# Kernel optimization log

Hardware: AMD Instinct MI355X
Metric: run time of the kernel (lower is better)

## Reference

```python
import jax, jax.numpy as jnp
import numpy as np

DIM = 256
K = 8192


def setup_inputs() -> dict:
    key = jax.random.key(0)
    k1, k2 = jax.random.split(key)
    x = jax.random.normal(k1, (16, DIM, 32, 32), dtype=jnp.float32)
    # embed buffer initialized uniform(-0.02, 0.02), shape (1, 1, dim, num_embeddings)
    embed = jax.random.uniform(k2, (1, 1, DIM, K), dtype=jnp.float32, minval=-0.02, maxval=0.02)
    return {"x": x, "embed": embed}


def reference(x, embed):
    B, C, H, W = x.shape
    K_ = embed.shape[-1]
    xp = jnp.transpose(x, (0, 2, 3, 1))            # [B,H,W,C]  (size=(1,1) => block reshape is identity)
    flat = xp.reshape(-1, C)                       # [N,C]
    e = embed.reshape(C, K_)                       # [C,K]
    # pairwise squared distances: ||f||^2 - 2 f.e + ||e||^2
    dist = (jnp.sum(flat * flat, axis=1, keepdims=True)
            - 2.0 * (flat @ e)
            + jnp.sum(e * e, axis=0, keepdims=True))  # [N,K]
    ind = jnp.argmin(dist, axis=1)                 # [N] (argmax of -dist)
    # codebook gather
    q = jnp.take(e.T, ind, axis=0).reshape(B, H, W, C)
    # perplexity from one-hot mean
    counts = jnp.zeros((K_,), dtype=jnp.float32).at[ind].add(1.0)
    avg_probs = counts / flat.shape[0]
    perplexity = jnp.exp(-jnp.sum(avg_probs * jnp.log(avg_probs + 1e-10)))
    # commitment loss (egu=False branch): mean((sg(q) - x)^2)
    diff = jnp.mean((jax.lax.stop_gradient(q) - xp) ** 2)
    # straight-through estimator
    q_st = xp + jax.lax.stop_gradient(q - xp)
    quantize = jnp.transpose(q_st, (0, 3, 1, 2))   # [B,C,H,W]
    embed_ind = ind.reshape(B, H, W)
    return quantize, diff, embed_ind, perplexity
```

## Files before the change

### kernel.cpp

```cpp
#include <hip/hip_runtime.h>

typedef _Float16 f16;
typedef f16 half8 __attribute__((ext_vector_type(8)));
typedef float f32x4 __attribute__((ext_vector_type(4)));
typedef unsigned long long u64;
typedef unsigned int u32;
typedef unsigned short u16;

#define KD 8192
#define DIFF_OFF 4194304
#define EIND_OFF 4194305
#define PERP_OFF 4210689
#define LCAP 262144
#define BUFSZ (24 * 512)


__device__ inline u32 umin32(u32 a, u32 b) { return a < b ? a : b; }
__device__ inline u32 umax32(u32 a, u32 b) { return a > b ? a : b; }
__device__ inline u64 pack64(float d, unsigned col) {
  u32 u = __float_as_uint(d);
  u = (u >> 31) ? ~u : (u | 0x80000000u);
  return ((u64)u << 32) | col;
}
__device__ inline void gl16(const f16* g, f16* l) {
  __builtin_amdgcn_global_load_lds(
      (const __attribute__((address_space(1))) void*)g,
      (__attribute__((address_space(3))) void*)l, 16, 0, 0);
}
__device__ inline float exact_d(const float* __restrict__ x, const float* __restrict__ e,
                                int b, int hw, int col, float F, const float* __restrict__ eev) {
  float a = 0.f;
#pragma unroll 8
  for (int c = 0; c < 256; ++c)
    a = fmaf(x[((size_t)(b * 256 + c) << 10) + hw], e[(size_t)c * KD + col], a);
  float t = fmaf(-2.f, a, F);
  return t + eev[col];
}

__global__ __launch_bounds__(256) void k_prep(const float* __restrict__ x,
                                              const float* __restrict__ e,
                                              float* __restrict__ Fv,
                                              float* __restrict__ eev,
                                              u32* __restrict__ eemax,
                                              f16* __restrict__ ehTf,
                                              f16* __restrict__ xhTf) {
#pragma clang fp contract(off)
  __shared__ float sm[64][65];
  const int bid = blockIdx.x, tid = threadIdx.x;
  if (bid < 32) {
    int k = bid * 256 + tid;
    float s = 0.0f;
    for (int c = 0; c < 256; ++c) { float v = e[(size_t)c * KD + k]; float sq = v * v; s = s + sq; }
    eev[k] = s;
    atomicMax(eemax, __float_as_uint(s));
  } else if (bid < 96) {
    int n = (bid - 32) * 256 + tid;
    int b = n >> 10, hw = n & 1023;
    const float* px = x + ((size_t)b << 18) + hw;
    float sblk[2];
#pragma unroll
    for (int blk = 0; blk < 2; ++blk) {
      float r[8];
#pragma unroll
      for (int j = 0; j < 8; ++j) { float v = px[(size_t)(blk * 128 + j) << 10]; r[j] = v * v; }
      for (int i = 8; i < 128; i += 8) {
#pragma unroll
        for (int j = 0; j < 8; ++j) {
          float v = px[(size_t)(blk * 128 + i + j) << 10];
          float sq = v * v;
          r[j] = r[j] + sq;
        }
      }
      sblk[blk] = ((r[0] + r[1]) + (r[2] + r[3])) + ((r[4] + r[5]) + (r[6] + r[7]));
    }
    Fv[n] = sblk[0] + sblk[1];
  } else if (bid < 608) {
    int t = bid - 96;
    int k0 = (t >> 2) * 64, c0 = (t & 3) * 64;
    int tx = tid & 63, ty = tid >> 6;
#pragma unroll
    for (int i = 0; i < 16; ++i) {
      int cl = i * 4 + ty;
      sm[cl][tx] = e[(size_t)(c0 + cl) * KD + k0 + tx];
    }
    __syncthreads();
#pragma unroll
    for (int p = 0; p < 2; ++p) {
      int i = tid + p * 256;
      int kl = i & 63, cg = i >> 6;
      int kkl = cg >> 2, gg = cg & 3;
      int chb = kkl * 32 + gg * 8;
      half8 h;
#pragma unroll
      for (int j = 0; j < 8; ++j) h[j] = (f16)sm[chb + j][kl];
      int tile = (k0 >> 4) + (kl >> 4);
      int kk = (c0 >> 5) + kkl;
      int lanef = gg * 16 + (kl & 15);
      *(half8*)(ehTf + ((size_t)(tile * 8 + kk) * 64 + lanef) * 8) = h;
    }
  } else {
    int t = bid - 608;
    int b = t >> 6, rem = t & 63;
    int hw0 = (rem >> 2) * 64, c0 = (rem & 3) * 64;
    int tx = tid & 63, ty = tid >> 6;
#pragma unroll
    for (int i = 0; i < 16; ++i) {
      int cl = i * 4 + ty;
      sm[cl][tx] = x[((size_t)(b * 256 + c0 + cl) << 10) + hw0 + tx];
    }
    __syncthreads();
#pragma unroll
    for (int p = 0; p < 2; ++p) {
      int i = tid + p * 256;
      int nl = i & 63, cg = i >> 6;
      int kkl = cg >> 2, gg = cg & 3;
      int chb = kkl * 32 + gg * 8;
      half8 h;
#pragma unroll
      for (int j = 0; j < 8; ++j) h[j] = (f16)sm[chb + j][nl];
      int rt = b * 64 + (hw0 >> 4) + (nl >> 4);
      int kk = (c0 >> 5) + kkl;
      int lanef = gg * 16 + (nl & 15);
      *(half8*)(xhTf + ((size_t)(rt * 8 + kk) * 64 + lanef) * 8) = h;
    }
  }
}

__global__ __launch_bounds__(512, 4) void k_gemm(const f16* __restrict__ xhTf,
                                                 const f16* __restrict__ ehTf,
                                                 const float* __restrict__ eev,
                                                 u32* __restrict__ m1,
                                                 u16* __restrict__ m2) {
  __shared__ __align__(16) f16 ldsbuf[3 * BUFSZ];
  __shared__ u32 red1[4][128];
  __shared__ u32 red2[4][128];
  const int tid = threadIdx.x;
  const int lane = tid & 63, w = tid >> 6;
  const int wm = w >> 2, wn = w & 3;
  const int l15 = lane & 15, g = lane >> 4;
  const int colblk = blockIdx.x & 31;
  const int rowblk = (int)blockIdx.x >> 5;

  const int blk0 = w * 3;
  const f16* gsrc[3];
#pragma unroll
  for (int i = 0; i < 3; ++i) {
    int b = blk0 + i;
    gsrc[i] = ((b < 8) ? (xhTf + (size_t)(rowblk * 8 + b) * 4096)
                       : (ehTf + (size_t)(colblk * 16 + (b - 8)) * 4096)) + lane * 8;
  }

  f32x4 acc[4][4];
#pragma unroll
  for (int i = 0; i < 4; ++i)
#pragma unroll
    for (int j = 0; j < 4; ++j) acc[i][j] = (f32x4){0.f, 0.f, 0.f, 0.f};

#pragma unroll
  for (int i = 0; i < 3; ++i) gl16(gsrc[i], ldsbuf + (blk0 + i) * 512);
#pragma unroll
  for (int i = 0; i < 3; ++i) gl16(gsrc[i] + 512, ldsbuf + BUFSZ + (blk0 + i) * 512);
  asm volatile("s_waitcnt vmcnt(3)" ::: "memory");
  __builtin_amdgcn_s_barrier();

  const f16* lrA = ldsbuf + (wm * 4) * 512 + lane * 8;
  const f16* lrB = ldsbuf + (8 + wn * 4) * 512 + lane * 8;

#pragma unroll
  for (int s = 0; s < 8; ++s) {
    const int cur = (s % 3) * BUFSZ;
    if (s < 6) {
      const int pre = ((s + 2) % 3) * BUFSZ;
#pragma unroll
      for (int i = 0; i < 3; ++i)
        gl16(gsrc[i] + (s + 2) * 512, ldsbuf + pre + (blk0 + i) * 512);
    }
    half8 af[4], bf[4];
#pragma unroll
    for (int mt = 0; mt < 4; ++mt) af[mt] = *(const half8*)(lrA + cur + mt * 512);
#pragma unroll
    for (int nt = 0; nt < 4; ++nt) bf[nt] = *(const half8*)(lrB + cur + nt * 512);
    __builtin_amdgcn_s_setprio(1);
#pragma unroll
    for (int mt = 0; mt < 4; ++mt)
#pragma unroll
      for (int nt = 0; nt < 4; ++nt)
        acc[mt][nt] = __builtin_amdgcn_mfma_f32_16x16x32_f16(af[mt], bf[nt], acc[mt][nt], 0, 0, 0);
    __builtin_amdgcn_s_setprio(0);
    if (s < 6) {
      asm volatile("s_waitcnt vmcnt(3)" ::: "memory");
      __builtin_amdgcn_s_barrier();
    } else if (s == 6) {
      asm volatile("s_waitcnt vmcnt(0)" ::: "memory");
      __builtin_amdgcn_s_barrier();
    }
  }

  float ee16[4];
#pragma unroll
  for (int nt = 0; nt < 4; ++nt)
    ee16[nt] = eev[colblk * 256 + wn * 64 + nt * 16 + l15] + 16.0f;
#pragma unroll
  for (int mt = 0; mt < 4; ++mt) {
#pragma unroll
    for (int r = 0; r < 4; ++r) {
      u32 s1 = 0xFFFFFFFFu, s2 = 0xFFFFFFFFu;
#pragma unroll
      for (int nt = 0; nt < 4; ++nt) {
        float d16 = fmaf(-2.f, acc[mt][nt][r], ee16[nt]);
        u32 k = (__float_as_uint(d16) & 0xFFFFFF00u) | (u32)(wn * 64 + nt * 16 + l15);
        u32 t = umax32(s1, k);
        s1 = umin32(s1, k);
        s2 = umin32(s2, t);
      }
#pragma unroll
      for (int msk = 1; msk < 16; msk <<= 1) {
        u32 o1 = (u32)__shfl_xor((int)s1, msk, 64);
        u32 o2 = (u32)__shfl_xor((int)s2, msk, 64);
        u32 t = umax32(s1, o1);
        s1 = umin32(s1, o1);
        s2 = umin32(umin32(s2, o2), t);
      }
      if (l15 == 0) {
        int rl = wm * 64 + mt * 16 + g * 4 + r;
        red1[wn][rl] = s1;
        red2[wn][rl] = s2;
      }
    }
  }
  __syncthreads();
  if (tid < 128) {
    u32 k1 = red1[0][tid], k2 = red2[0][tid];
#pragma unroll
    for (int wv = 1; wv < 4; ++wv) {
      u32 a = red1[wv][tid], b2 = red2[wv][tid];
      u32 t = umax32(k1, a);
      k1 = umin32(k1, a);
      k2 = umin32(k2, umin32(t, b2));
    }
    int row = rowblk * 128 + tid;
    m1[(size_t)colblk * 16384 + row] = k1;
    float d2 = __uint_as_float(k2 & 0xFFFFFF00u);
    float tq = fmaxf(fminf(d2 * 2048.0f, 65535.f), 0.f);
    m2[(size_t)colblk * 16384 + row] = (u16)(u32)tq;
  }
}

__global__ __launch_bounds__(256) void k_sel(const float* __restrict__ x,
                                             const float* __restrict__ e,
                                             const u32* __restrict__ m1,
                                             const u16* __restrict__ m2,
                                             const float* __restrict__ Fv,
                                             const float* __restrict__ eev,
                                             const u32* __restrict__ eemax,
                                             u64* __restrict__ best,
                                             u32* __restrict__ cnt,
                                             u32* __restrict__ list) {
  const int row = blockIdx.x * 4 + (threadIdx.x >> 6);
  const int lane = threadIdx.x & 63;
  u32 m1v = 0xFFFFFFFFu;
  u32 m2v = 0xFFFFu;
  if (lane < 32) {
    m1v = m1[(size_t)lane * 16384 + row];
    m2v = (u32)m2[(size_t)lane * 16384 + row];
  }
  u32 gk = m1v;
#pragma unroll
  for (int msk = 1; msk < 64; msk <<= 1) gk = umin32(gk, (u32)__shfl_xor((int)gk, msk, 64));
  const float F = Fv[row];
  const float eps = 0x1p-9f * sqrtf(F * __uint_as_float(*eemax)) + 4e-4f;
  const float thr = (__uint_as_float(gk & 0xFFFFFF00u) - 16.0f) + 2.f * eps + 1e-3f;

  const bool f1 = (lane < 32) && (__uint_as_float(m1v & 0xFFFFFF00u) - 16.0f <= thr);
  const bool trig = (lane < 32) && ((float)m2v * (1.0f / 2048.0f) - 16.0f <= thr);
  const u64 bal = __ballot(f1);
  const bool anyt = __any(trig);

  const int col = lane * 256 + (int)(m1v & 255u);
  const int b = row >> 10, hw = row & 1023;

  if (__popcll(bal) == 1 && !anyt) {
    if (f1) best[row] = (u64)(unsigned)col;
  } else {
    if (f1) {
      float d = exact_d(x, e, b, hw, col, F, eev);
      atomicMin(&best[row], pack64(d, (unsigned)col));
    }
    if (trig) {
      u32 slot = atomicAdd(cnt, 1u);
      if (slot < LCAP) list[slot] = (u32)((row << 5) | lane);
      else {
        for (int j = 0; j < 256; ++j) {
          int cj = lane * 256 + j;
          float d = exact_d(x, e, b, hw, cj, F, eev);
          atomicMin(&best[row], pack64(d, (unsigned)cj));
        }
      }
    }
  }
}

__global__ __launch_bounds__(256) void k_chunk(const float* __restrict__ x,
                                               const float* __restrict__ e,
                                               const float* __restrict__ Fv,
                                               const float* __restrict__ eev,
                                               const u32* __restrict__ cnt,
                                               const u32* __restrict__ list,
                                               u64* __restrict__ best) {
  u32 n = *cnt; if (n > LCAP) n = LCAP;
  const int lane = threadIdx.x & 63;
  for (u32 t = blockIdx.x * 4 + (threadIdx.x >> 6); t < n; t += gridDim.x * 4) {
    u32 v = list[t];
    int row = (int)(v >> 5), cb = (int)(v & 31u);
    int b = row >> 10, hw = row & 1023;
    float F = Fv[row];
    int base = cb * 256 + lane;
    float a0 = 0.f, a1 = 0.f, a2 = 0.f, a3 = 0.f;
#pragma unroll 8
    for (int c = 0; c < 256; ++c) {
      float xv = x[((size_t)(b * 256 + c) << 10) + hw];
      const float* ep = e + (size_t)c * KD + base;
      a0 = fmaf(xv, ep[0], a0);
      a1 = fmaf(xv, ep[64], a1);
      a2 = fmaf(xv, ep[128], a2);
      a3 = fmaf(xv, ep[192], a3);
    }
    float acc4[4] = {a0, a1, a2, a3};
#pragma unroll
    for (int q = 0; q < 4; ++q) {
      int col = base + q * 64;
      float t2 = fmaf(-2.f, acc4[q], F);
      float d = t2 + eev[col];
      atomicMin(&best[row], pack64(d, (unsigned)col));
    }
  }
}

__global__ __launch_bounds__(256) void k_ind(const u64* __restrict__ best,
                                             u16* __restrict__ idx16,
                                             int* __restrict__ counts,
                                             float* __restrict__ out) {
  int n = blockIdx.x * 256 + threadIdx.x;
  u32 idx = (u32)(best[n] & 0xFFFFFFFFull);
  idx16[n] = (u16)idx;
  out[EIND_OFF + n] = (float)idx;
  atomicAdd(&counts[idx], 1);
}

__global__ __launch_bounds__(256) void k_out(const float* __restrict__ x,
                                             const float* __restrict__ e,
                                             const u16* __restrict__ idx16,
                                             float* __restrict__ out,
                                             float* __restrict__ dpart) {
  __shared__ float sd[256];
  int tid = threadIdx.x;
  float local = 0.0f;
  for (size_t v = (size_t)blockIdx.x * 256 + tid; v < 1048576ull; v += 262144ull) {
    size_t i = v * 4;
    int hw = (int)(i & 1023);
    int c = (int)((i >> 10) & 255);
    int bb = (int)(i >> 18);
    int n = (bb << 10) + hw;
    ushort4 id4 = *(const ushort4*)(idx16 + n);
    float4 xv = *(const float4*)(x + i);
    const float* ec = e + (size_t)c * KD;
    float d0 = ec[id4.x] - xv.x;
    float d1 = ec[id4.y] - xv.y;
    float d2 = ec[id4.z] - xv.z;
    float d3 = ec[id4.w] - xv.w;
    float4 o = {xv.x + d0, xv.y + d1, xv.z + d2, xv.w + d3};
    *(float4*)(out + i) = o;
    local += d0 * d0 + d1 * d1 + d2 * d2 + d3 * d3;
  }
  sd[tid] = local;
  __syncthreads();
  for (int s = 128; s > 0; s >>= 1) {
    if (tid < s) sd[tid] += sd[tid + s];
    __syncthreads();
  }
  if (tid == 0) dpart[blockIdx.x] = sd[0];
}

__global__ __launch_bounds__(256) void k_perp(const int* __restrict__ counts,
                                              const float* __restrict__ dpart,
                                              float* __restrict__ out) {
  __shared__ float sd[256];
  int tid = threadIdx.x;
  float s = 0.0f;
  for (int k = tid; k < KD; k += 256) {
    float p = (float)counts[k] * (1.0f / 16384.0f);
    s += p * logf(p + 1e-10f);
  }
  sd[tid] = s;
  __syncthreads();
  for (int t = 128; t > 0; t >>= 1) {
    if (tid < t) sd[tid] += sd[tid + t];
    __syncthreads();
  }
  float S = sd[0];
  __syncthreads();
  float d = 0.0f;
  for (int t = tid; t < 1024; t += 256) d += dpart[t];
  sd[tid] = d;
  __syncthreads();
  for (int t = 128; t > 0; t >>= 1) {
    if (tid < t) sd[tid] += sd[tid + t];
    __syncthreads();
  }
  if (tid == 0) {
    out[DIFF_OFF] = sd[0] * (1.0f / 4194304.0f);
    out[PERP_OFF] = expf(-S);
  }
}

extern "C" void kernel_launch(void* const* d_in, const int* in_sizes, int n_in,
                              void* d_out, int out_size, void* d_ws, size_t ws_size,
                              hipStream_t stream) {
  const float* x = (const float*)d_in[0];
  const float* e = (const float*)d_in[1];
  float* out = (float*)d_out;
  char* dc = (char*)d_out;
  char* ws = (char*)d_ws;

  u64* best = (u64*)(ws);
  float* Fv = (float*)(ws + 131072);
  float* eev = (float*)(ws + 196608);
  u16* idx16 = (u16*)(ws + 229376);
  int* counts = (int*)(ws + 262144);
  float* dpart = (float*)(ws + 294912);
  u32* eemax = (u32*)(ws + 299008);
  u32* cnt = (u32*)(ws + 299012);

  f16* ehTf = (f16*)(dc);
  f16* xhTf = (f16*)(dc + 4194304);
  u32* m1 = (u32*)(dc + 12582912);
  u16* m2 = (u16*)(dc + 14680064);
  u32* list = (u32*)(dc + 15728640);

  hipMemsetAsync(best, 0xFF, 131072, stream);
  hipMemsetAsync(counts, 0, 36872, stream);

  k_prep<<<1632, 256, 0, stream>>>(x, e, Fv, eev, eemax, ehTf, xhTf);
  k_gemm<<<4096, 512, 0, stream>>>(xhTf, ehTf, eev, m1, m2);
  k_sel<<<4096, 256, 0, stream>>>(x, e, m1, m2, Fv, eev, eemax, best, cnt, list);
  k_chunk<<<1024, 256, 0, stream>>>(x, e, Fv, eev, cnt, list, best);
  k_ind<<<64, 256, 0, stream>>>(best, idx16, counts, out);
  k_out<<<1024, 256, 0, stream>>>(x, e, idx16, out, dpart);
  k_perp<<<1, 256, 0, stream>>>(counts, dpart, out);
}
```

Before: 224.1 us.

## Make GEMM blocks persistent over four column tiles with continuous prefetch pipeline

Each GEMM block now processes four consecutive 256-column tiles instead of one, with the triple-buffered global-to-LDS pipeline running across all 32 K-steps so loads for the next tile overlap the current tile's epilogue. Block count drops fourfold, ee values are staged once into LDS, and the per-tile top-2 reduction runs inside the loop with extra barriers. This removes per-block prologue and pipeline-drain costs but lowers the number of blocks available for scheduling and adds barriers in the epilogue.

```diff
diff --git a/kernel.cpp b/kernel.cpp
--- a/kernel.cpp
+++ b/kernel.cpp
@@ -132,23 +132,31 @@
                                                  u32* __restrict__ m1,
                                                  u16* __restrict__ m2) {
   __shared__ __align__(16) f16 ldsbuf[3 * BUFSZ];
+  __shared__ float eelds[1024];
   __shared__ u32 red1[4][128];
   __shared__ u32 red2[4][128];
   const int tid = threadIdx.x;
   const int lane = tid & 63, w = tid >> 6;
   const int wm = w >> 2, wn = w & 3;
   const int l15 = lane & 15, g = lane >> 4;
-  const int colblk = blockIdx.x & 31;
-  const int rowblk = (int)blockIdx.x >> 5;
-
+  const int cg = blockIdx.x & 7;
+  const int rowblk = (int)blockIdx.x >> 3;
   const int blk0 = w * 3;
-  const f16* gsrc[3];
-#pragma unroll
-  for (int i = 0; i < 3; ++i) {
-    int b = blk0 + i;
-    gsrc[i] = ((b < 8) ? (xhTf + (size_t)(rowblk * 8 + b) * 4096)
-                       : (ehTf + (size_t)(colblk * 16 + (b - 8)) * 4096)) + lane * 8;
-  }
+
+  eelds[tid] = eev[cg * 1024 + tid] + 16.0f;
+  eelds[tid + 512] = eev[cg * 1024 + 512 + tid] + 16.0f;
+
+  auto stage = [&](int gs, int buf) {
+    const int s = gs & 7, cb = gs >> 3;
+#pragma unroll
+    for (int i = 0; i < 3; ++i) {
+      const int b = blk0 + i;
+      const f16* src = (b < 8)
+          ? xhTf + (size_t)(rowblk * 8 + b) * 4096 + s * 512
+          : ehTf + (size_t)((cg * 4 + cb) * 16 + (b - 8)) * 4096 + s * 512;
+      gl16(src + lane * 8, ldsbuf + buf * BUFSZ + (blk0 + i) * 512);
+    }
+  };
 
   f32x4 acc[4][4];
 #pragma unroll
@@ -156,25 +164,18 @@
 #pragma unroll
     for (int j = 0; j < 4; ++j) acc[i][j] = (f32x4){0.f, 0.f, 0.f, 0.f};
 
-#pragma unroll
-  for (int i = 0; i < 3; ++i) gl16(gsrc[i], ldsbuf + (blk0 + i) * 512);
-#pragma unroll
-  for (int i = 0; i < 3; ++i) gl16(gsrc[i] + 512, ldsbuf + BUFSZ + (blk0 + i) * 512);
+  stage(0, 0);
+  stage(1, 1);
   asm volatile("s_waitcnt vmcnt(3)" ::: "memory");
+  asm volatile("s_waitcnt lgkmcnt(0)" ::: "memory");
   __builtin_amdgcn_s_barrier();
 
   const f16* lrA = ldsbuf + (wm * 4) * 512 + lane * 8;
   const f16* lrB = ldsbuf + (8 + wn * 4) * 512 + lane * 8;
 
-#pragma unroll
-  for (int s = 0; s < 8; ++s) {
-    const int cur = (s % 3) * BUFSZ;
-    if (s < 6) {
-      const int pre = ((s + 2) % 3) * BUFSZ;
-#pragma unroll
-      for (int i = 0; i < 3; ++i)
-        gl16(gsrc[i] + (s + 2) * 512, ldsbuf + pre + (blk0 + i) * 512);
-    }
+  for (int gs = 0; gs < 32; ++gs) {
+    const int cur = (gs % 3) * BUFSZ;
+    if (gs < 30) stage(gs + 2, (gs + 2) % 3);
     half8 af[4], bf[4];
 #pragma unroll
     for (int mt = 0; mt < 4; ++mt) af[mt] = *(const half8*)(lrA + cur + mt * 512);
@@ -187,62 +188,73 @@
       for (int nt = 0; nt < 4; ++nt)
         acc[mt][nt] = __builtin_amdgcn_mfma_f32_16x16x32_f16(af[mt], bf[nt], acc[mt][nt], 0, 0, 0);
     __builtin_amdgcn_s_setprio(0);
-    if (s < 6) {
+    if (gs < 30) {
       asm volatile("s_waitcnt vmcnt(3)" ::: "memory");
       __builtin_amdgcn_s_barrier();
-    } else if (s == 6) {
+    } else if (gs == 30) {
       asm volatile("s_waitcnt vmcnt(0)" ::: "memory");
       __builtin_amdgcn_s_barrier();
     }
-  }
-
-  float ee16[4];
-#pragma unroll
-  for (int nt = 0; nt < 4; ++nt)
-    ee16[nt] = eev[colblk * 256 + wn * 64 + nt * 16 + l15] + 16.0f;
-#pragma unroll
-  for (int mt = 0; mt < 4; ++mt) {
-#pragma unroll
-    for (int r = 0; r < 4; ++r) {
-      u32 s1 = 0xFFFFFFFFu, s2 = 0xFFFFFFFFu;
-#pragma unroll
-      for (int nt = 0; nt < 4; ++nt) {
-        float d16 = fmaf(-2.f, acc[mt][nt][r], ee16[nt]);
-        u32 k = (__float_as_uint(d16) & 0xFFFFFF00u) | (u32)(wn * 64 + nt * 16 + l15);
-        u32 t = umax32(s1, k);
-        s1 = umin32(s1, k);
-        s2 = umin32(s2, t);
+
+    if ((gs & 7) == 7) {
+      const int cbl = gs >> 3;
+      const int colblk = cg * 4 + cbl;
+      float ee16[4];
+#pragma unroll
+      for (int nt = 0; nt < 4; ++nt)
+        ee16[nt] = eelds[cbl * 256 + wn * 64 + nt * 16 + l15];
+#pragma unroll
+      for (int mt = 0; mt < 4; ++mt) {
+#pragma unroll
+        for (int r = 0; r < 4; ++r) {
+          u32 s1 = 0xFFFFFFFFu, s2 = 0xFFFFFFFFu;
+#pragma unroll
+          for (int nt = 0; nt < 4; ++nt) {
+            float d16 = fmaf(-2.f, acc[mt][nt][r], ee16[nt]);
+            u32 k = (__float_as_uint(d16) & 0xFFFFFF00u) | (u32)(wn * 64 + nt * 16 + l15);
+            u32 t = umax32(s1, k);
+            s1 = umin32(s1, k);
+            s2 = umin32(s2, t);
+          }
+#pragma unroll
+          for (int msk = 1; msk < 16; msk <<= 1) {
+            u32 o1 = (u32)__shfl_xor((int)s1, msk, 64);
+            u32 o2 = (u32)__shfl_xor((int)s2, msk, 64);
+            u32 t = umax32(s1, o1);
+            s1 = umin32(s1, o1);
+            s2 = umin32(umin32(s2, o2), t);
+          }
+          if (l15 == 0) {
+            int rl = wm * 64 + mt * 16 + g * 4 + r;
+            red1[wn][rl] = s1;
+            red2[wn][rl] = s2;
+          }
+        }
       }
-#pragma unroll
-      for (int msk = 1; msk < 16; msk <<= 1) {
-        u32 o1 = (u32)__shfl_xor((int)s1, msk, 64);
-        u32 o2 = (u32)__shfl_xor((int)s2, msk, 64);
-        u32 t = umax32(s1, o1);
-        s1 = umin32(s1, o1);
-        s2 = umin32(umin32(s2, o2), t);
+      asm volatile("s_waitcnt lgkmcnt(0)" ::: "memory");
+      __builtin_amdgcn_s_barrier();
+      if (tid < 128) {
+        u32 k1 = red1[0][tid], k2 = red2[0][tid];
+#pragma unroll
+        for (int wv = 1; wv < 4; ++wv) {
+          u32 a = red1[wv][tid], b2 = red2[wv][tid];
+          u32 t = umax32(k1, a);
+          k1 = umin32(k1, a);
+          k2 = umin32(k2, umin32(t, b2));
+        }
+        int row = rowblk * 128 + tid;
+        m1[(size_t)colblk * 16384 + row] = k1;
+        float d2 = __uint_as_float(k2 & 0xFFFFFF00u);
+        float tq = fmaxf(fminf(d2 * 2048.0f, 65535.f), 0.f);
+        m2[(size_t)colblk * 16384 + row] = (u16)(u32)tq;
       }
-      if (l15 == 0) {
-        int rl = wm * 64 + mt * 16 + g * 4 + r;
-        red1[wn][rl] = s1;
-        red2[wn][rl] = s2;
-      }
-    }
-  }
-  __syncthreads();
-  if (tid < 128) {
-    u32 k1 = red1[0][tid], k2 = red2[0][tid];
-#pragma unroll
-    for (int wv = 1; wv < 4; ++wv) {
-      u32 a = red1[wv][tid], b2 = red2[wv][tid];
-      u32 t = umax32(k1, a);
-      k1 = umin32(k1, a);
-      k2 = umin32(k2, umin32(t, b2));
-    }
-    int row = rowblk * 128 + tid;
-    m1[(size_t)colblk * 16384 + row] = k1;
-    float d2 = __uint_as_float(k2 & 0xFFFFFF00u);
-    float tq = fmaxf(fminf(d2 * 2048.0f, 65535.f), 0.f);
-    m2[(size_t)colblk * 16384 + row] = (u16)(u32)tq;
+      asm volatile("s_waitcnt lgkmcnt(0)" ::: "memory");
+      __builtin_amdgcn_s_barrier();
+#pragma unroll
+      for (int i = 0; i < 4; ++i)
+#pragma unroll
+        for (int j = 0; j < 4; ++j) acc[i][j] = (f32x4){0.f, 0.f, 0.f, 0.f};
+    }
   }
 }
 
@@ -441,7 +453,7 @@
   hipMemsetAsync(counts, 0, 36872, stream);
 
   k_prep<<<1632, 256, 0, stream>>>(x, e, Fv, eev, eemax, ehTf, xhTf);
-  k_gemm<<<4096, 512, 0, stream>>>(xhTf, ehTf, eev, m1, m2);
+  k_gemm<<<1024, 512, 0, stream>>>(xhTf, ehTf, eev, m1, m2);
   k_sel<<<4096, 256, 0, stream>>>(x, e, m1, m2, Fv, eev, eemax, best, cnt, list);
   k_chunk<<<1024, 256, 0, stream>>>(x, e, Fv, eev, cnt, list, best);
   k_ind<<<64, 256, 0, stream>>>(best, idx16, counts, out);
```

New measurement: 233.8 us. 1.04x slower.
